# Performance work log

Measured on AMD Instinct MI355X. Metric: run time of the kernel, lower is better.

The kernel has to match this reference:

```python
import jax, jax.numpy as jnp
import numpy as np

EPS = 1e-05


def _rms_norm(x, w):
    xf = x.astype(jnp.float32)
    o = xf * jax.lax.rsqrt(jnp.square(xf).mean(-1, keepdims=True) + EPS)
    return (o * w.astype(jnp.float32)).astype(x.dtype)


def _apply_rope(x, sin, cos):
    # x: [B,T,N,H]; sin/cos: [B,T,H/2]
    half = x.shape[-1] // 2
    x1, x2 = x[..., :half], x[..., half:]
    s, c = sin[:, :, None, :], cos[:, :, None, :]
    return jnp.concatenate([x1 * c - x2 * s, x2 * c + x1 * s], axis=-1).astype(x.dtype)


def setup_inputs() -> dict:
    key = jax.random.key(0)
    ks = jax.random.split(key, 12)
    B, T, D, FF, HALF = 2, 1024, 4096, 12288, 64
    return {
        "x": jax.random.normal(ks[0], (B, T, D), jnp.float32),
        "sin": jax.random.uniform(ks[1], (B, T, HALF), jnp.float32),
        "cos": jax.random.uniform(ks[2], (B, T, HALF), jnp.float32),
        "attn_norm_w": jax.random.uniform(ks[3], (D,), jnp.float32),
        "ff_norm_w": jax.random.uniform(ks[4], (D,), jnp.float32),
        "wq": jax.random.normal(ks[5], (D, D), jnp.float32) * 0.02,
        "wk": jax.random.normal(ks[6], (D, D), jnp.float32) * 0.02,
        "wv": jax.random.normal(ks[7], (D, D), jnp.float32) * 0.02,
        "wo": jax.random.normal(ks[8], (D, D), jnp.float32) * 0.02,
        "w_ff": jax.random.normal(ks[9], (D, FF), jnp.float32) * 0.02,
        "w_up": jax.random.normal(ks[10], (D, FF), jnp.float32) * 0.02,
        "w_out": jax.random.normal(ks[11], (FF, D), jnp.float32) * 0.02,
    }


def reference(x, sin, cos, attn_norm_w, ff_norm_w, wq, wk, wv, wo, w_ff, w_up, w_out):
    B, T, D = x.shape
    head_dim = sin.shape[-1] * 2  # 128
    # --- attention ---
    xn = _rms_norm(x, attn_norm_w)
    q = (xn @ wq).reshape(B, T, -1, head_dim)
    k = (xn @ wk).reshape(B, T, -1, head_dim)
    v = (xn @ wv).reshape(B, T, -1, head_dim)
    q = _apply_rope(q, sin, cos)
    k = _apply_rope(k, sin, cos)
    scale = jnp.asarray(1.0 / np.sqrt(head_dim), dtype=q.dtype)
    logits = jnp.einsum("BTNH,BSNH->BNTS", q, k) * scale
    probs = jax.nn.softmax(logits.astype(jnp.float32), axis=-1).astype(k.dtype)
    attn = jnp.einsum("BNTS,BSNH->BTNH", probs, v).reshape(B, T, D)
    x = x + attn @ wo
    # --- SwiGLU MLP ---
    res = x
    xn = _rms_norm(x, ff_norm_w)
    h = jax.nn.silu(xn @ w_ff) * (xn @ w_up)
    return res + h @ w_out
```

## Files before the change

### kernel.cpp

```cpp
#include <hip/hip_runtime.h>
#include <type_traits>


#define D_MODEL 4096
#define FF_DIM  12288
#define SEQ     1024
#define NBATCH  2
#define M_ROWS  2048
#define NHEAD   32
#define HDIM    128
#define QKV_N   12288
#define FF2_N   24576

typedef short bf16x8 __attribute__((ext_vector_type(8)));
typedef ushort u16x16 __attribute__((ext_vector_type(16)));
typedef float f32x4  __attribute__((ext_vector_type(4)));

__device__ __forceinline__ ushort f2bf(float f) {
  unsigned u = __float_as_uint(f);
  u += 0x7FFFu + ((u >> 16) & 1u);
  return (ushort)(u >> 16);
}
__device__ __forceinline__ float bf2f(ushort u) {
  return __uint_as_float(((unsigned)u) << 16);
}

__device__ __forceinline__ void gload_lds16(const ushort* gsrc, ushort* ldst) {
  __builtin_amdgcn_global_load_lds((const __attribute__((address_space(1))) void*)gsrc,
                                   (__attribute__((address_space(3))) void*)ldst, 16, 0, 0);
}

#define SBAR()   asm volatile("s_barrier" ::: "memory")
#define LGKM0()  asm volatile("s_waitcnt lgkmcnt(0)" ::: "memory")
#define VMCNT8() asm volatile("s_waitcnt vmcnt(8)" ::: "memory")

__global__ __launch_bounds__(256)
void transpose_convert(const float* __restrict__ W, ushort* __restrict__ Wt,
                       int K, int N, int remap, int upoff)
{
  __shared__ float tile[64][68];
  const int t = threadIdx.x;
  const size_t k0 = (size_t)blockIdx.y * 64, n0 = (size_t)blockIdx.x * 64;
  const int lx = (t & 15) * 4, ly = t >> 4;
#pragma unroll
  for (int i = 0; i < 64; i += 16)
    *(float4*)&tile[ly + i][lx] = *(const float4*)&W[(k0 + ly + i) * N + n0 + lx];
  __syncthreads();
  const int n = t >> 2, kq = (t & 3) * 16;
  u16x16 ov;
#pragma unroll
  for (int e = 0; e < 16; e++) ov[e] = f2bf(tile[kq + e][n]);
  size_t nOut = n0 + n;
  if (remap) nOut = ((nOut >> 7) << 8) + (nOut & 127) + upoff;
  *(u16x16*)&Wt[nOut * K + k0 + kq] = ov;
}

__global__ __launch_bounds__(256)
void v_transpose(const ushort* __restrict__ v, ushort* __restrict__ vt)
{
  __shared__ ushort tile[32][33];
  const int x = threadIdx.x, y = threadIdx.y;
  const int row0 = blockIdx.x * 32;
  const int d0 = blockIdx.y * 32;
  const int h = blockIdx.z;
  const int b = row0 >> 10, sl0 = row0 & (SEQ - 1);
#pragma unroll
  for (int i = 0; i < 32; i += 8)
    tile[y + i][x] = v[(size_t)(row0 + y + i) * QKV_N + h * HDIM + d0 + x];
  __syncthreads();
  ushort* ob = vt + ((size_t)(b * NHEAD + h) * HDIM + d0) * SEQ + sl0;
#pragma unroll
  for (int i = 0; i < 32; i += 8)
    ob[(size_t)(y + i) * SEQ + x] = tile[x][y + i];
}

__global__ __launch_bounds__(256)
void rmsnorm_kernel(const float* __restrict__ x, const float* __restrict__ w,
                    ushort* __restrict__ out)
{
  const int row = blockIdx.x, t = threadIdx.x;
  const float* xr = x + (size_t)row * D_MODEL;
  float4 vv[4];
  float ss = 0.f;
#pragma unroll
  for (int p = 0; p < 4; p++) {
    vv[p] = *(const float4*)&xr[p * 1024 + t * 4];
    ss += vv[p].x * vv[p].x + vv[p].y * vv[p].y + vv[p].z * vv[p].z + vv[p].w * vv[p].w;
  }
#pragma unroll
  for (int mm = 1; mm < 64; mm <<= 1) ss += __shfl_xor(ss, mm);
  __shared__ float wsum[4];
  if ((t & 63) == 0) wsum[t >> 6] = ss;
  __syncthreads();
  ss = wsum[0] + wsum[1] + wsum[2] + wsum[3];
  const float rs = rsqrtf(ss * (1.f / 4096.f) + 1e-5f);
#pragma unroll
  for (int p = 0; p < 4; p++) {
    const float4 wv = *(const float4*)&w[p * 1024 + t * 4];
    ushort4 ov;
    ov.x = f2bf(vv[p].x * rs * wv.x);
    ov.y = f2bf(vv[p].y * rs * wv.y);
    ov.z = f2bf(vv[p].z * rs * wv.z);
    ov.w = f2bf(vv[p].w * rs * wv.w);
    *(ushort4*)&out[(size_t)row * D_MODEL + p * 1024 + t * 4] = ov;
  }
}

__global__ __launch_bounds__(256)
void rope_kernel(ushort* __restrict__ q, ushort* __restrict__ k,
                 const float* __restrict__ sinp, const float* __restrict__ cosp,
                 int ld)
{
  const size_t idx = (size_t)blockIdx.x * 256 + threadIdx.x;
  const int d = (int)(idx & 63);
  const int h = (int)((idx >> 6) & 31);
  const int t = (int)(idx >> 11);
  const float s = sinp[t * 64 + d], c = cosp[t * 64 + d];
  const size_t base = (size_t)t * ld + h * HDIM + d;
  const float q1 = bf2f(q[base]), q2 = bf2f(q[base + 64]);
  q[base]      = f2bf(q1 * c - q2 * s);
  q[base + 64] = f2bf(q2 * c + q1 * s);
  const float k1 = bf2f(k[base]), k2 = bf2f(k[base + 64]);
  k[base]      = f2bf(k1 * c - k2 * s);
  k[base + 64] = f2bf(k2 * c + k1 * s);
}

__global__ __launch_bounds__(64)
void attn_fwd(const ushort* __restrict__ q, const ushort* __restrict__ k,
              const ushort* __restrict__ vt, ushort* __restrict__ o,
              int ldq, int ldo)
{
  const int l = threadIdx.x, c16 = l & 15, g = l >> 4;
  const int qt = blockIdx.x, h = blockIdx.y, b = blockIdx.z;
  __shared__ __align__(16) ushort P_lds[16 * 32];

  const size_t head_off = (size_t)h * HDIM;
  const size_t rowQ = (size_t)(b * SEQ + qt * 16 + c16);
  const ushort* vtb = vt + (size_t)(b * NHEAD + h) * HDIM * SEQ;
  bf16x8 qf[4];
#pragma unroll
  for (int kc = 0; kc < 4; kc++)
    qf[kc] = *(const bf16x8*)(q + rowQ * ldq + head_off + kc * 32 + g * 8);

  f32x4 oacc[8];
#pragma unroll
  for (int i = 0; i < 8; i++) oacc[i] = (f32x4){0.f, 0.f, 0.f, 0.f};
  float mrow[4] = {-1e30f, -1e30f, -1e30f, -1e30f};
  float lrow[4] = {0.f, 0.f, 0.f, 0.f};
  const float scale = 0.08838834764831845f;
  const float L2E = 1.4426950408889634f;

  for (int s0 = 0; s0 < SEQ; s0 += 32) {
    f32x4 st[2];
#pragma unroll
    for (int t = 0; t < 2; t++) {
      f32x4 a = (f32x4){0.f, 0.f, 0.f, 0.f};
      const ushort* kb = k + (size_t)(b * SEQ + s0 + t * 16 + c16) * ldq + head_off + g * 8;
#pragma unroll
      for (int kc = 0; kc < 4; kc++) {
        bf16x8 kf = *(const bf16x8*)(kb + kc * 32);
        a = __builtin_amdgcn_mfma_f32_16x16x32_bf16(qf[kc], kf, a, 0, 0, 0);
      }
      st[t] = a;
    }
    float a4s[4], mn4[4], p0v[4], p1v[4];
#pragma unroll
    for (int r = 0; r < 4; r++) {
      const float s0v = st[0][r] * scale, s1v = st[1][r] * scale;
      float cm = fmaxf(s0v, s1v);
#pragma unroll
      for (int mm = 1; mm < 16; mm <<= 1) cm = fmaxf(cm, __shfl_xor(cm, mm));
      const float mn = fmaxf(mrow[r], cm);
      a4s[r] = exp2f((mrow[r] - mn) * L2E);
      mn4[r] = mn;
      p0v[r] = exp2f((s0v - mn) * L2E);
      p1v[r] = exp2f((s1v - mn) * L2E);
    }
    const f32x4 av = (f32x4){a4s[0], a4s[1], a4s[2], a4s[3]};
    const float aprod = a4s[0] * a4s[1] * a4s[2] * a4s[3];
    if (__any(aprod != 1.0f)) {
#pragma unroll
      for (int dbi = 0; dbi < 8; dbi++) oacc[dbi] *= av;
    }
#pragma unroll
    for (int r = 0; r < 4; r++) {
      float rsum = p0v[r] + p1v[r];
#pragma unroll
      for (int mm = 1; mm < 16; mm <<= 1) rsum += __shfl_xor(rsum, mm);
      lrow[r] = lrow[r] * a4s[r] + rsum;
      mrow[r] = mn4[r];
      P_lds[(g * 4 + r) * 32 + c16]      = f2bf(p0v[r]);
      P_lds[(g * 4 + r) * 32 + 16 + c16] = f2bf(p1v[r]);
    }
    __syncthreads();
    const bf16x8 pf = *(const bf16x8*)&P_lds[c16 * 32 + g * 8];
#pragma unroll
    for (int dbi = 0; dbi < 8; dbi++) {
      const bf16x8 vf = *(const bf16x8*)(vtb + (size_t)(dbi * 16 + c16) * SEQ + s0 + g * 8);
      oacc[dbi] = __builtin_amdgcn_mfma_f32_16x16x32_bf16(pf, vf, oacc[dbi], 0, 0, 0);
    }
    __syncthreads();
  }
  const size_t rowO = (size_t)(b * SEQ + qt * 16 + g * 4);
#pragma unroll
  for (int dbi = 0; dbi < 8; dbi++)
#pragma unroll
    for (int r = 0; r < 4; r++)
      o[(rowO + r) * ldo + head_off + dbi * 16 + c16] = f2bf(oacc[dbi][r] / lrow[r]);
}

__global__ __launch_bounds__(256)
void add3_kernel(const float* __restrict__ a, const float* __restrict__ b,
                 const float* __restrict__ c, float* __restrict__ d, int n4)
{
  for (int i = blockIdx.x * 256 + threadIdx.x; i < n4; i += gridDim.x * 256) {
    const float4 av = ((const float4*)a)[i];
    const float4 bv = ((const float4*)b)[i];
    const float4 cv = ((const float4*)c)[i];
    float4 dv;
    dv.x = av.x + bv.x + cv.x; dv.y = av.y + bv.y + cv.y;
    dv.z = av.z + bv.z + cv.z; dv.w = av.w + bv.w + cv.w;
    ((float4*)d)[i] = dv;
  }
}

template <int EPI, bool SPLITK>
__global__ __launch_bounds__(512, 2)
void gemm8p(const ushort* __restrict__ A, const ushort* __restrict__ Bt,
            const float* __restrict__ res, void* __restrict__ Cout,
            int M, int N, int Ks, int ldk)
{
  __shared__ __align__(16) ushort lds[65536];
  const int tid = threadIdx.x;
  const int w = tid >> 6, l = tid & 63;
  const int c16 = l & 15, g = l >> 4;
  const int wr = w >> 2, wc = w & 3;

  const int nwg = gridDim.x;
  const int q8 = nwg >> 3, r8 = nwg & 7;
  const int xcd = blockIdx.x & 7, loc = blockIdx.x >> 3;
  int wg = (xcd < r8 ? xcd * (q8 + 1) : r8 * (q8 + 1) + (xcd - r8) * q8) + loc;
  int kslice = 0;
  if constexpr (SPLITK) { kslice = wg >> 7; wg &= 127; }
  const size_t m0 = (size_t)(wg & 7) * 256;
  const size_t n0 = (size_t)(wg >> 3) * 256;
  const int nk = Ks >> 6;

  const int srow  = (w << 3) + (l >> 3);
  const int scolE = ((l & 7) ^ (l >> 3)) << 3;
  const ushort* gA = A  + (size_t)kslice * Ks + (m0 + srow) * (size_t)ldk + scolE;
  const ushort* gB = Bt + (size_t)kslice * Ks + (n0 + srow) * (size_t)ldk + scolE;

#define STG_A(p, h, q, tk)                                                        \
  gload_lds16(gA + (size_t)((h) * 128 + (q) * 64) * ldk + (size_t)(tk) * 64,      \
              lds + (p) * 16384 + (h) * 8192 + (q) * 4096 + (w << 9))
#define STG_B(p, h, q, tk)                                                        \
  gload_lds16(gB + (size_t)((h) * 128 + (q) * 64) * ldk + (size_t)(tk) * 64,      \
              lds + 32768 + (p) * 16384 + (h) * 8192 + (q) * 4096 + (w << 9))
#define STG_A2(p, h, tk) do { STG_A(p, h, 0, tk); STG_A(p, h, 1, tk); } while (0)
#define STG_B2(p, h, tk) do { STG_B(p, h, 0, tk); STG_B(p, h, 1, tk); } while (0)

  const int xorE = (c16 & 7) << 3;
  const int k0E = (g * 8) ^ xorE;
  const int k1E = (32 + g * 8) ^ xorE;
  const int aRow = wr * 64 + c16;
  const int bRow = wc * 32 + c16;

  const char* ldsb = (const char*)lds;
  const char* pA0 = ldsb + aRow * 128 + k0E * 2;
  const char* pA1 = ldsb + aRow * 128 + k1E * 2;
  const char* pB0 = ldsb + 65536 + bRow * 128 + k0E * 2;
  const char* pB1 = ldsb + 65536 + bRow * 128 + k1E * 2;

#define RDA(P, qm, i, kk)                                                         \
  (*(const bf16x8*)((kk ? pA1 : pA0) + (P) * 32768 + (qm) * 16384 + (i) * 2048))
#define RDB(P, qn, j, kk)                                                         \
  (*(const bf16x8*)((kk ? pB1 : pB0) + (P) * 32768 + (qn) * 16384 + (j) * 2048))

  f32x4 acc[8][4];
#pragma unroll
  for (int i = 0; i < 8; i++)
#pragma unroll
    for (int j = 0; j < 4; j++) acc[i][j] = (f32x4){0.f, 0.f, 0.f, 0.f};
  bf16x8 a[4][2], b0[2][2], b1[2][2];

  STG_A2(0, 0, 0); STG_A2(0, 1, 0); STG_B2(0, 0, 0); STG_B2(0, 1, 0);
  STG_A2(1, 0, 1); STG_A2(1, 1, 1); STG_B2(1, 0, 1); STG_B2(1, 1, 1);
  VMCNT8(); SBAR();

  auto tileBody = [&](auto Pc, int t) {
    constexpr int P = decltype(Pc)::value;
    const int tn2 = (t + 2 < nk) ? t + 2 : t + 2 - nk;

#pragma unroll
    for (int j = 0; j < 2; ++j) { b0[j][0] = RDB(P, 0, j, 0); b0[j][1] = RDB(P, 0, j, 1); }
#pragma unroll
    for (int i = 0; i < 4; ++i) { a[i][0] = RDA(P, 0, i, 0); a[i][1] = RDA(P, 0, i, 1); }
    SBAR(); LGKM0();
    __builtin_amdgcn_s_setprio(1);
#pragma unroll
    for (int i = 0; i < 4; ++i)
#pragma unroll
      for (int j = 0; j < 2; ++j)
#pragma unroll
        for (int kk = 0; kk < 2; ++kk)
          acc[i][j] = __builtin_amdgcn_mfma_f32_16x16x32_bf16(a[i][kk], b0[j][kk], acc[i][j], 0, 0, 0);
    __builtin_amdgcn_s_setprio(0);
    SBAR();

#pragma unroll
    for (int j = 0; j < 2; ++j) { b1[j][0] = RDB(P, 1, j, 0); b1[j][1] = RDB(P, 1, j, 1); }
    STG_A2(P, 0, tn2);
    STG_B2(P, 0, tn2);
    SBAR(); LGKM0();
    __builtin_amdgcn_s_setprio(1);
#pragma unroll
    for (int i = 0; i < 4; ++i)
#pragma unroll
      for (int j = 0; j < 2; ++j)
#pragma unroll
        for (int kk = 0; kk < 2; ++kk)
          acc[i][2 + j] = __builtin_amdgcn_mfma_f32_16x16x32_bf16(a[i][kk], b1[j][kk], acc[i][2 + j], 0, 0, 0);
    __builtin_amdgcn_s_setprio(0);
    SBAR();

#pragma unroll
    for (int i = 0; i < 4; ++i) { a[i][0] = RDA(P, 1, i, 0); a[i][1] = RDA(P, 1, i, 1); }
    STG_B2(P, 1, tn2);
    SBAR(); LGKM0();
    __builtin_amdgcn_s_setprio(1);
#pragma unroll
    for (int i = 0; i < 4; ++i)
#pragma unroll
      for (int j = 0; j < 2; ++j)
#pragma unroll
        for (int kk = 0; kk < 2; ++kk)
          acc[4 + i][j] = __builtin_amdgcn_mfma_f32_16x16x32_bf16(a[i][kk], b0[j][kk], acc[4 + i][j], 0, 0, 0);
    __builtin_amdgcn_s_setprio(0);
    SBAR();

    STG_A2(P, 1, tn2);
    SBAR(); LGKM0();
    __builtin_amdgcn_s_setprio(1);
#pragma unroll
    for (int i = 0; i < 4; ++i)
#pragma unroll
      for (int j = 0; j < 2; ++j)
#pragma unroll
        for (int kk = 0; kk < 2; ++kk)
          acc[4 + i][2 + j] = __builtin_amdgcn_mfma_f32_16x16x32_bf16(a[i][kk], b1[j][kk], acc[4 + i][2 + j], 0, 0, 0);
    __builtin_amdgcn_s_setprio(0);
    VMCNT8(); SBAR();
  };

  for (int t = 0; t < nk; t += 2) {
    tileBody(std::integral_constant<int, 0>{}, t);
    tileBody(std::integral_constant<int, 1>{}, t + 1);
  }

#pragma unroll
  for (int qm = 0; qm < 2; qm++)
#pragma unroll
    for (int i = 0; i < 4; i++)
#pragma unroll
      for (int qn = 0; qn < 2; qn++)
#pragma unroll
        for (int j = 0; j < 2; j++)
#pragma unroll
          for (int r = 0; r < 4; r++) {
            const size_t row = m0 + qm * 128 + wr * 64 + i * 16 + g * 4 + r;
            if constexpr (EPI == 2) {
              if (qn == 1) continue;
              const float hv = acc[qm * 4 + i][j][r];
              const float uv = acc[qm * 4 + i][2 + j][r];
              const size_t col = (n0 >> 1) + wc * 32 + j * 16 + c16;
              ((ushort*)Cout)[row * (size_t)(N >> 1) + col] =
                  f2bf((hv / (1.f + __expf(-hv))) * uv);
            } else {
              const size_t col = n0 + qn * 128 + wc * 32 + j * 16 + c16;
              const size_t idx = row * N + col;
              const float v = acc[qm * 4 + i][qn * 2 + j][r];
              if constexpr (EPI == 0)      ((ushort*)Cout)[idx] = f2bf(v);
              else if constexpr (EPI == 1) ((float*)Cout)[idx] = res[idx] + v;
              else                         ((float*)Cout)[(size_t)kslice * M * N + idx] = v;
            }
          }
#undef STG_A
#undef STG_B
#undef STG_A2
#undef STG_B2
#undef RDA
#undef RDB
}

extern "C" void kernel_launch(void* const* d_in, const int* in_sizes, int n_in,
                              void* d_out, int out_size, void* d_ws, size_t ws_size,
                              hipStream_t stream)
{
  const float* x    = (const float*)d_in[0];
  const float* sinp = (const float*)d_in[1];
  const float* cosp = (const float*)d_in[2];
  const float* anw  = (const float*)d_in[3];
  const float* fnw  = (const float*)d_in[4];
  const float* wq   = (const float*)d_in[5];
  const float* wk   = (const float*)d_in[6];
  const float* wv   = (const float*)d_in[7];
  const float* wo   = (const float*)d_in[8];
  const float* wff  = (const float*)d_in[9];
  const float* wup  = (const float*)d_in[10];
  const float* wout = (const float*)d_in[11];
  float* out = (float*)d_out;

  const size_t szDD   = (size_t)D_MODEL * D_MODEL * 2;
  const size_t szDF   = (size_t)D_MODEL * FF_DIM * 2;
  const size_t szAct2 = (size_t)M_ROWS * D_MODEL * 2;
  const size_t szAct4 = (size_t)M_ROWS * D_MODEL * 4;
  const size_t szQKV  = (size_t)M_ROWS * QKV_N * 2;
  const size_t MN     = (size_t)M_ROWS * D_MODEL;

  char* ws = (char*)d_ws;
  size_t off = 0;
  auto alloc = [&](size_t bytes) -> char* {
    char* p = ws + off;
    off += (bytes + 255) & ~(size_t)255;
    return p;
  };
  ushort* R1    = (ushort*)alloc(szDF);
  ushort* R2    = (ushort*)alloc(2 * szDF);
  ushort* wot   = (ushort*)alloc(szDD);
  ushort* xn    = (ushort*)alloc(szAct2);
  ushort* qkv   = (ushort*)alloc(szQKV);
  ushort* attnb = (ushort*)alloc(szAct2);
  float*  x2    = (float*)alloc(szAct4);
  ushort* vtb   = (ushort*)alloc(szAct2);
  float*  part  = (float*)alloc(2 * MN * 4);
  if (off > ws_size) return;

  transpose_convert<<<dim3(D_MODEL / 64, D_MODEL / 64), 256, 0, stream>>>(wq, R1, D_MODEL, D_MODEL, 0, 0);
  transpose_convert<<<dim3(D_MODEL / 64, D_MODEL / 64), 256, 0, stream>>>(wk, R1 + (size_t)D_MODEL * D_MODEL, D_MODEL, D_MODEL, 0, 0);
  transpose_convert<<<dim3(D_MODEL / 64, D_MODEL / 64), 256, 0, stream>>>(wv, R1 + 2 * (size_t)D_MODEL * D_MODEL, D_MODEL, D_MODEL, 0, 0);
  transpose_convert<<<dim3(D_MODEL / 64, D_MODEL / 64), 256, 0, stream>>>(wo, wot, D_MODEL, D_MODEL, 0, 0);
  transpose_convert<<<dim3(FF_DIM / 64, D_MODEL / 64), 256, 0, stream>>>(wff, R2, D_MODEL, FF_DIM, 1, 0);
  transpose_convert<<<dim3(FF_DIM / 64, D_MODEL / 64), 256, 0, stream>>>(wup, R2, D_MODEL, FF_DIM, 1, 128);

  rmsnorm_kernel<<<M_ROWS, 256, 0, stream>>>(x, anw, xn);
  gemm8p<0, false><<<(M_ROWS / 256) * (QKV_N / 256), 512, 0, stream>>>(xn, R1, nullptr, qkv, M_ROWS, QKV_N, D_MODEL, D_MODEL);
  transpose_convert<<<dim3(D_MODEL / 64, FF_DIM / 64), 256, 0, stream>>>(wout, R1, FF_DIM, D_MODEL, 0, 0);
  rope_kernel<<<(M_ROWS * NHEAD * 64) / 256, 256, 0, stream>>>(qkv, qkv + D_MODEL, sinp, cosp, QKV_N);
  v_transpose<<<dim3(M_ROWS / 32, HDIM / 32, NHEAD), dim3(32, 8), 0, stream>>>(qkv + 2 * D_MODEL, vtb);
  attn_fwd<<<dim3(SEQ / 16, NHEAD, NBATCH), 64, 0, stream>>>(qkv, qkv + D_MODEL, vtb, attnb, QKV_N, D_MODEL);
  gemm8p<3, true><<<256, 512, 0, stream>>>(attnb, wot, nullptr, part, M_ROWS, D_MODEL, D_MODEL / 2, D_MODEL);
  add3_kernel<<<2048, 256, 0, stream>>>(x, part, part + MN, x2, (int)(MN / 4));

  rmsnorm_kernel<<<M_ROWS, 256, 0, stream>>>(x2, fnw, xn);
  gemm8p<2, false><<<(M_ROWS / 256) * (FF2_N / 256), 512, 0, stream>>>(xn, R2, nullptr, qkv , M_ROWS, FF2_N, D_MODEL, D_MODEL);
  gemm8p<3, true><<<256, 512, 0, stream>>>(qkv, R1, nullptr, part, M_ROWS, D_MODEL, FF_DIM / 2, FF_DIM);
  add3_kernel<<<2048, 256, 0, stream>>>(x2, part, part + MN, out, (int)(MN / 4));
}
```

Measured before the change: 1.353 ms.

## Process two query tiles per attention wavefront with lazy max rescaling

The attention kernel now handles 32 query rows per 64-thread block as two 16-row tiles, so each K and V fragment loaded from memory feeds twice as many MFMAs. It also skips the running-max update and accumulator rescale unless some score exceeds the stored max by more than a threshold, and it defers the cross-lane row-sum reduction to the end. The grid is halved, which reduces parallelism across CUs and raises register pressure. The lazy rescale allows unnormalized exponents up to about e^8 before correction.

```diff
diff --git a/kernel.cpp b/kernel.cpp
--- a/kernel.cpp
+++ b/kernel.cpp
@@ -132,81 +132,127 @@
 {
   const int l = threadIdx.x, c16 = l & 15, g = l >> 4;
   const int qt = blockIdx.x, h = blockIdx.y, b = blockIdx.z;
-  __shared__ __align__(16) ushort P_lds[16 * 32];
+  __shared__ __align__(16) ushort P_lds[2][16 * 32];
 
   const size_t head_off = (size_t)h * HDIM;
-  const size_t rowQ = (size_t)(b * SEQ + qt * 16 + c16);
   const ushort* vtb = vt + (size_t)(b * NHEAD + h) * HDIM * SEQ;
-  bf16x8 qf[4];
-#pragma unroll
-  for (int kc = 0; kc < 4; kc++)
-    qf[kc] = *(const bf16x8*)(q + rowQ * ldq + head_off + kc * 32 + g * 8);
-
-  f32x4 oacc[8];
-#pragma unroll
-  for (int i = 0; i < 8; i++) oacc[i] = (f32x4){0.f, 0.f, 0.f, 0.f};
-  float mrow[4] = {-1e30f, -1e30f, -1e30f, -1e30f};
-  float lrow[4] = {0.f, 0.f, 0.f, 0.f};
+  bf16x8 qf[2][4];
+#pragma unroll
+  for (int tile = 0; tile < 2; tile++) {
+    const size_t rowQ = (size_t)(b * SEQ + qt * 32 + tile * 16 + c16);
+#pragma unroll
+    for (int kc = 0; kc < 4; kc++)
+      qf[tile][kc] = *(const bf16x8*)(q + rowQ * ldq + head_off + kc * 32 + g * 8);
+  }
+
+  f32x4 oacc[2][8];
+#pragma unroll
+  for (int tile = 0; tile < 2; tile++)
+#pragma unroll
+    for (int i = 0; i < 8; i++) oacc[tile][i] = (f32x4){0.f, 0.f, 0.f, 0.f};
+  float mrow[2][4], lsum[2][4];
+#pragma unroll
+  for (int tile = 0; tile < 2; tile++)
+#pragma unroll
+    for (int r = 0; r < 4; r++) { mrow[tile][r] = -1e30f; lsum[tile][r] = 0.f; }
   const float scale = 0.08838834764831845f;
   const float L2E = 1.4426950408889634f;
 
   for (int s0 = 0; s0 < SEQ; s0 += 32) {
-    f32x4 st[2];
+    bf16x8 kfr[2][4];
 #pragma unroll
     for (int t = 0; t < 2; t++) {
-      f32x4 a = (f32x4){0.f, 0.f, 0.f, 0.f};
       const ushort* kb = k + (size_t)(b * SEQ + s0 + t * 16 + c16) * ldq + head_off + g * 8;
 #pragma unroll
-      for (int kc = 0; kc < 4; kc++) {
-        bf16x8 kf = *(const bf16x8*)(kb + kc * 32);
-        a = __builtin_amdgcn_mfma_f32_16x16x32_bf16(qf[kc], kf, a, 0, 0, 0);
+      for (int kc = 0; kc < 4; kc++) kfr[t][kc] = *(const bf16x8*)(kb + kc * 32);
+    }
+    f32x4 st[2][2];
+#pragma unroll
+    for (int tile = 0; tile < 2; tile++)
+#pragma unroll
+      for (int t = 0; t < 2; t++) {
+        f32x4 a = (f32x4){0.f, 0.f, 0.f, 0.f};
+#pragma unroll
+        for (int kc = 0; kc < 4; kc++)
+          a = __builtin_amdgcn_mfma_f32_16x16x32_bf16(qf[tile][kc], kfr[t][kc], a, 0, 0, 0);
+        st[tile][t] = a;
       }
-      st[t] = a;
-    }
-    float a4s[4], mn4[4], p0v[4], p1v[4];
-#pragma unroll
-    for (int r = 0; r < 4; r++) {
-      const float s0v = st[0][r] * scale, s1v = st[1][r] * scale;
-      float cm = fmaxf(s0v, s1v);
-#pragma unroll
-      for (int mm = 1; mm < 16; mm <<= 1) cm = fmaxf(cm, __shfl_xor(cm, mm));
-      const float mn = fmaxf(mrow[r], cm);
-      a4s[r] = exp2f((mrow[r] - mn) * L2E);
-      mn4[r] = mn;
-      p0v[r] = exp2f((s0v - mn) * L2E);
-      p1v[r] = exp2f((s1v - mn) * L2E);
-    }
-    const f32x4 av = (f32x4){a4s[0], a4s[1], a4s[2], a4s[3]};
-    const float aprod = a4s[0] * a4s[1] * a4s[2] * a4s[3];
-    if (__any(aprod != 1.0f)) {
-#pragma unroll
-      for (int dbi = 0; dbi < 8; dbi++) oacc[dbi] *= av;
-    }
-#pragma unroll
-    for (int r = 0; r < 4; r++) {
-      float rsum = p0v[r] + p1v[r];
-#pragma unroll
-      for (int mm = 1; mm < 16; mm <<= 1) rsum += __shfl_xor(rsum, mm);
-      lrow[r] = lrow[r] * a4s[r] + rsum;
-      mrow[r] = mn4[r];
-      P_lds[(g * 4 + r) * 32 + c16]      = f2bf(p0v[r]);
-      P_lds[(g * 4 + r) * 32 + 16 + c16] = f2bf(p1v[r]);
+
+    float s0v[2][4], s1v[2][4];
+    float worst = -1e30f;
+#pragma unroll
+    for (int tile = 0; tile < 2; tile++)
+#pragma unroll
+      for (int r = 0; r < 4; r++) {
+        s0v[tile][r] = st[tile][0][r] * scale;
+        s1v[tile][r] = st[tile][1][r] * scale;
+        worst = fmaxf(worst, fmaxf(s0v[tile][r], s1v[tile][r]) - mrow[tile][r]);
+      }
+
+    if (__any(worst > 8.0f)) {
+#pragma unroll
+      for (int tile = 0; tile < 2; tile++) {
+        float a4[4];
+#pragma unroll
+        for (int r = 0; r < 4; r++) {
+          float cm = fmaxf(s0v[tile][r], s1v[tile][r]);
+#pragma unroll
+          for (int mm = 1; mm < 16; mm <<= 1) cm = fmaxf(cm, __shfl_xor(cm, mm));
+          const float mn = fmaxf(mrow[tile][r], cm);
+          a4[r] = exp2f((mrow[tile][r] - mn) * L2E);
+          mrow[tile][r] = mn;
+          const float p0 = exp2f((s0v[tile][r] - mn) * L2E);
+          const float p1 = exp2f((s1v[tile][r] - mn) * L2E);
+          lsum[tile][r] = lsum[tile][r] * a4[r] + p0 + p1;
+          P_lds[tile][(g * 4 + r) * 32 + c16]      = f2bf(p0);
+          P_lds[tile][(g * 4 + r) * 32 + 16 + c16] = f2bf(p1);
+        }
+        const f32x4 av = (f32x4){a4[0], a4[1], a4[2], a4[3]};
+#pragma unroll
+        for (int dbi = 0; dbi < 8; dbi++) oacc[tile][dbi] *= av;
+      }
+    } else {
+#pragma unroll
+      for (int tile = 0; tile < 2; tile++)
+#pragma unroll
+        for (int r = 0; r < 4; r++) {
+          const float p0 = exp2f((s0v[tile][r] - mrow[tile][r]) * L2E);
+          const float p1 = exp2f((s1v[tile][r] - mrow[tile][r]) * L2E);
+          lsum[tile][r] += p0 + p1;
+          P_lds[tile][(g * 4 + r) * 32 + c16]      = f2bf(p0);
+          P_lds[tile][(g * 4 + r) * 32 + 16 + c16] = f2bf(p1);
+        }
     }
     __syncthreads();
-    const bf16x8 pf = *(const bf16x8*)&P_lds[c16 * 32 + g * 8];
+    const bf16x8 pf0 = *(const bf16x8*)&P_lds[0][c16 * 32 + g * 8];
+    const bf16x8 pf1 = *(const bf16x8*)&P_lds[1][c16 * 32 + g * 8];
 #pragma unroll
     for (int dbi = 0; dbi < 8; dbi++) {
       const bf16x8 vf = *(const bf16x8*)(vtb + (size_t)(dbi * 16 + c16) * SEQ + s0 + g * 8);
-      oacc[dbi] = __builtin_amdgcn_mfma_f32_16x16x32_bf16(pf, vf, oacc[dbi], 0, 0, 0);
+      oacc[0][dbi] = __builtin_amdgcn_mfma_f32_16x16x32_bf16(pf0, vf, oacc[0][dbi], 0, 0, 0);
+      oacc[1][dbi] = __builtin_amdgcn_mfma_f32_16x16x32_bf16(pf1, vf, oacc[1][dbi], 0, 0, 0);
     }
     __syncthreads();
   }
-  const size_t rowO = (size_t)(b * SEQ + qt * 16 + g * 4);
-#pragma unroll
-  for (int dbi = 0; dbi < 8; dbi++)
-#pragma unroll
-    for (int r = 0; r < 4; r++)
-      o[(rowO + r) * ldo + head_off + dbi * 16 + c16] = f2bf(oacc[dbi][r] / lrow[r]);
+
+#pragma unroll
+  for (int tile = 0; tile < 2; tile++)
+#pragma unroll
+    for (int r = 0; r < 4; r++) {
+#pragma unroll
+      for (int mm = 1; mm < 16; mm <<= 1)
+        lsum[tile][r] += __shfl_xor(lsum[tile][r], mm);
+    }
+#pragma unroll
+  for (int tile = 0; tile < 2; tile++) {
+    const size_t rowO = (size_t)(b * SEQ + qt * 32 + tile * 16 + g * 4);
+#pragma unroll
+    for (int dbi = 0; dbi < 8; dbi++)
+#pragma unroll
+      for (int r = 0; r < 4; r++)
+        o[(rowO + r) * ldo + head_off + dbi * 16 + c16] =
+            f2bf(oacc[tile][dbi][r] / lsum[tile][r]);
+  }
 }
 
 __global__ __launch_bounds__(256)
@@ -448,7 +494,7 @@
   transpose_convert<<<dim3(D_MODEL / 64, FF_DIM / 64), 256, 0, stream>>>(wout, R1, FF_DIM, D_MODEL, 0, 0);
   rope_kernel<<<(M_ROWS * NHEAD * 64) / 256, 256, 0, stream>>>(qkv, qkv + D_MODEL, sinp, cosp, QKV_N);
   v_transpose<<<dim3(M_ROWS / 32, HDIM / 32, NHEAD), dim3(32, 8), 0, stream>>>(qkv + 2 * D_MODEL, vtb);
-  attn_fwd<<<dim3(SEQ / 16, NHEAD, NBATCH), 64, 0, stream>>>(qkv, qkv + D_MODEL, vtb, attnb, QKV_N, D_MODEL);
+  attn_fwd<<<dim3(SEQ / 32, NHEAD, NBATCH), 64, 0, stream>>>(qkv, qkv + D_MODEL, vtb, attnb, QKV_N, D_MODEL);
   gemm8p<3, true><<<256, 512, 0, stream>>>(attnb, wot, nullptr, part, M_ROWS, D_MODEL, D_MODEL / 2, D_MODEL);
   add3_kernel<<<2048, 256, 0, stream>>>(x, part, part + MN, x2, (int)(MN / 4));
 
```

New measurement: 1.307 ms. 1.04x faster.
